# Kernel optimization log

Measured on AMD Instinct MI355X. Metric: run time of the kernel, lower is better.

## Reference

```python
import jax, jax.numpy as jnp
import numpy as np

EPS = 1e-5

def _gn(x, w, b):
    # GroupNorm with 1 group on [N, C]: normalize each row over C, then affine.
    mu = jnp.mean(x, axis=-1, keepdims=True)
    var = jnp.mean((x - mu) ** 2, axis=-1, keepdims=True)
    return (x - mu) * jax.lax.rsqrt(var + EPS) * w + b

def setup_inputs() -> dict:
    key = jax.random.key(0)
    ks = jax.random.split(key, 24)
    N_AGT, N_CTX, E, D, NC = 50000, 100000, 500000, 128, 2
    s = 0.05  # weight init scale
    inp = {
        "agts": jax.random.normal(ks[0], (N_AGT, D), jnp.float32),
        "ctx": jax.random.normal(ks[1], (N_CTX, D), jnp.float32),
        "agt_ctrs": jax.random.normal(ks[2], (N_AGT, NC), jnp.float32),
        "ctx_ctrs": jax.random.normal(ks[3], (N_CTX, NC), jnp.float32),
        "hi": jax.random.randint(ks[4], (E,), 0, N_AGT, jnp.int32),
        "wi": jax.random.randint(ks[5], (E,), 0, N_CTX, jnp.int32),
        # dist MLP: Linear(2->128, bias) + ReLU, then Linear(128->128 no bias)+GN+ReLU
        "Wd1": jax.random.normal(ks[6], (D, NC), jnp.float32) * s,
        "bd1": jnp.zeros((D,), jnp.float32),
        "Wd2": jax.random.normal(ks[7], (D, D), jnp.float32) * s,
        "gd2w": jnp.ones((D,), jnp.float32), "gd2b": jnp.zeros((D,), jnp.float32),
        # query: Linear(128->128 no bias)+GN+ReLU
        "Wq": jax.random.normal(ks[8], (D, D), jnp.float32) * s,
        "gqw": jnp.ones((D,), jnp.float32), "gqb": jnp.zeros((D,), jnp.float32),
        # ctx MLP: Linear(384->128 no bias)+GN+ReLU, then Linear(128->128 no bias)
        "Wc1": jax.random.normal(ks[9], (D, 3 * D), jnp.float32) * s,
        "gc1w": jnp.ones((D,), jnp.float32), "gc1b": jnp.zeros((D,), jnp.float32),
        "Wc2": jax.random.normal(ks[10], (D, D), jnp.float32) * s,
        # agt linear (no bias), post-scatter GN, final Linear(no bias)+GN
        "Wa": jax.random.normal(ks[11], (D, D), jnp.float32) * s,
        "gnw": jnp.ones((D,), jnp.float32), "gnb": jnp.zeros((D,), jnp.float32),
        "Wl": jax.random.normal(ks[12], (D, D), jnp.float32) * s,
        "glw": jnp.ones((D,), jnp.float32), "glb": jnp.zeros((D,), jnp.float32),
    }
    return inp

def reference(agts, ctx, agt_ctrs, ctx_ctrs, hi, wi,
              Wd1, bd1, Wd2, gd2w, gd2b, Wq, gqw, gqb,
              Wc1, gc1w, gc1b, Wc2, Wa, gnw, gnb, Wl, glw, glb):
    res = agts
    # dist branch: relative center offsets of edges -> MLP
    d = agt_ctrs[hi] - ctx_ctrs[wi]                    # [E, 2]
    d = jax.nn.relu(d @ Wd1.T + bd1)                   # [E, 128]
    d = jax.nn.relu(_gn(d @ Wd2.T, gd2w, gd2b))        # [E, 128]
    # query branch: gathered agent features
    q = jax.nn.relu(_gn(agts[hi] @ Wq.T, gqw, gqb))    # [E, 128]
    # ctx branch: concat(dist, query, gathered ctx) -> MLP
    c = jnp.concatenate([d, q, ctx[wi]], axis=1)       # [E, 384]
    c = jax.nn.relu(_gn(c @ Wc1.T, gc1w, gc1b))        # [E, 128]
    c = c @ Wc2.T                                      # [E, 128]
    # scatter-add messages back to agents
    a = agts @ Wa.T
    a = a.at[hi].add(c)
    a = jax.nn.relu(_gn(a, gnw, gnb))
    a = _gn(a @ Wl.T, glw, glb)
    return jax.nn.relu(a + res)
```

## Files before the change

### kernel.cpp

```cpp
#include <hip/hip_runtime.h>
#include <hip/hip_bf16.h>

#define D 128
#define TM 64
#define APITCH 136
#define WSLICE 16384

typedef __attribute__((ext_vector_type(8))) short short8;
typedef __attribute__((ext_vector_type(4))) float f32x4;
typedef __attribute__((ext_vector_type(2))) float f32x2;

__device__ __forceinline__ short f2bf(float f) {
    union { float f; unsigned u; } v; v.f = f;
    unsigned r = v.u + 0x7fffu + ((v.u >> 16) & 1u);
    return (short)(r >> 16);
}
__device__ __forceinline__ float bflo(unsigned v) {
    union { unsigned u; float f; } t; t.u = v << 16; return t.f;
}
__device__ __forceinline__ float bfhi(unsigned v) {
    union { unsigned u; float f; } t; t.u = v & 0xffff0000u; return t.f;
}
__device__ __forceinline__ unsigned pkbf(float a, float b) {
    return (unsigned)(unsigned short)f2bf(a) | ((unsigned)(unsigned short)f2bf(b) << 16);
}

struct TileLDS {
    short A[TM * APITCH];
    f32x2 red[TM][4][4];
    f32x2 mr[TM];
    int hi_s[TM];
    int wi_s[TM];
};

struct WPA { const float* src[8]; int pitch[8]; int coloff[8]; };

__global__ __launch_bounds__(256)
void k_wprep(WPA a, short* __restrict__ wf) {
    int slice = blockIdx.x & 7, chunk = blockIdx.x >> 3;
    int tid = threadIdx.x, lane = tid & 63;
    int slot = chunk * 4 + (tid >> 6);
    int w = slot >> 3, t = (slot >> 2) & 1, ks = slot & 3;
    int lr = lane & 15, kh = lane >> 4;
    const float* src = a.src[slice];
    int row = w * 32 + t * 16 + lr;
    int col0 = a.coloff[slice] + ks * 32 + kh * 8;
    short8 v;
#pragma unroll
    for (int j = 0; j < 8; ++j) v[j] = f2bf(src[(size_t)row * a.pitch[slice] + col0 + j]);
    *(short8*)&wf[(size_t)slice * WSLICE + ((size_t)slot * 64 + lane) * 8] = v;
}

__device__ __forceinline__ void load_wset_pre(const short* wf, int slice, int w, int lane,
                                              short8 frag[2][4]) {
    const short8* p = (const short8*)(wf + (size_t)slice * WSLICE);
#pragma unroll
    for (int t = 0; t < 2; ++t)
#pragma unroll
        for (int ks = 0; ks < 4; ++ks)
            frag[t][ks] = p[((w * 2 + t) * 4 + ks) * 64 + lane];
}

__device__ __forceinline__ void wave_gemm(const short* A, const short8 frag[2][4],
                                          int lr, int kh, f32x4 acc[4][2]) {
#pragma unroll
    for (int mt = 0; mt < 4; ++mt)
#pragma unroll
        for (int t = 0; t < 2; ++t)
            acc[mt][t] = (f32x4){0.f, 0.f, 0.f, 0.f};
#pragma unroll
    for (int ks = 0; ks < 4; ++ks) {
        short8 a[4];
#pragma unroll
        for (int mt = 0; mt < 4; ++mt)
            a[mt] = *(const short8*)&A[(mt * 16 + lr) * APITCH + ks * 32 + kh * 8];
#pragma unroll
        for (int mt = 0; mt < 4; ++mt)
#pragma unroll
            for (int t = 0; t < 2; ++t)
                acc[mt][t] = __builtin_amdgcn_mfma_f32_16x16x32_bf16(a[mt], frag[t][ks], acc[mt][t], 0, 0, 0);
    }
}

__device__ __forceinline__ void store_acc_global(float* Y, long rbase, int M,
                                                 const f32x4 acc[4][2], int lane, int w) {
    int lr = lane & 15, hh = lane >> 4;
#pragma unroll
    for (int mt = 0; mt < 4; ++mt)
#pragma unroll
        for (int t = 0; t < 2; ++t)
#pragma unroll
            for (int r = 0; r < 4; ++r) {
                int row = mt * 16 + hh * 4 + r;
                if (rbase + row < M)
                    Y[(size_t)(rbase + row) * D + w * 32 + t * 16 + lr] = acc[mt][t][r];
            }
}

__device__ __forceinline__ void store_acc_pk(unsigned* Y, long rbase, int M,
                                             const f32x4 acc[4][2], int lane, int w) {
    int lr = lane & 15, hh = lane >> 4;
#pragma unroll
    for (int mt = 0; mt < 4; ++mt)
#pragma unroll
        for (int r = 0; r < 4; ++r) {
            int row = mt * 16 + hh * 4 + r;
            if (rbase + row < M)
                Y[(size_t)(rbase + row) * 64 + w * 16 + lr] = pkbf(acc[mt][0][r], acc[mt][1][r]);
        }
}

__device__ __forceinline__ void gn_stats(TileLDS& L, const f32x4 acc[4][2],
                                         int tid, int lane, int w) {
    int lr = lane & 15, hh = lane >> 4;
#pragma unroll
    for (int mt = 0; mt < 4; ++mt)
#pragma unroll
        for (int r = 0; r < 4; ++r) {
            float s = acc[mt][0][r] + acc[mt][1][r];
            float q = acc[mt][0][r] * acc[mt][0][r] + acc[mt][1][r] * acc[mt][1][r];
            s += __shfl_xor(s, 1); q += __shfl_xor(q, 1);
            s += __shfl_xor(s, 2); q += __shfl_xor(q, 2);
            if ((lr & 3) == mt) {
                int row = mt * 16 + hh * 4 + r;
                L.red[row][w][lr >> 2] = (f32x2){s, q};
            }
        }
    __syncthreads();
    if (tid < TM) {
        float s = 0.f, q = 0.f;
        const f32x2* p = (const f32x2*)L.red[tid];
#pragma unroll
        for (int i = 0; i < 16; ++i) { f32x2 v = p[i]; s += v[0]; q += v[1]; }
        float mu = s * (1.f / 128.f);
        float var = q * (1.f / 128.f) - mu * mu;
        L.mr[tid] = (f32x2){mu, rsqrtf(var + 1e-5f)};
    }
    __syncthreads();
}

__device__ __forceinline__ void gn_reg(TileLDS& L, const f32x4 acc[4][2],
                                       float gw0, float gb0, float gw1, float gb1,
                                       int tid, int lane, int w) {
    gn_stats(L, acc, tid, lane, w);
    int lr = lane & 15, hh = lane >> 4, n0 = w * 32;
#pragma unroll
    for (int mt = 0; mt < 4; ++mt)
#pragma unroll
        for (int r = 0; r < 4; ++r) {
            int row = mt * 16 + hh * 4 + r;
            f32x2 m = L.mr[row];
            float v0 = (acc[mt][0][r] - m[0]) * m[1] * gw0 + gb0;
            float v1 = (acc[mt][1][r] - m[0]) * m[1] * gw1 + gb1;
            L.A[row * APITCH + n0 + lr]      = f2bf(fmaxf(v0, 0.f));
            L.A[row * APITCH + n0 + 16 + lr] = f2bf(fmaxf(v1, 0.f));
        }
    __syncthreads();
}

__device__ __forceinline__ void stage_rows_to_A(TileLDS& L, const float* X, long rbase, int M, int tid) {
#pragma unroll
    for (int it = 0; it < 8; ++it) {
        int chunk = tid + it * 256;
        int row = chunk >> 5, c4 = chunk & 31;
        long r = rbase + row;
        float4 v = (r < M) ? *(const float4*)&X[(size_t)r * D + c4 * 4] : make_float4(0.f, 0.f, 0.f, 0.f);
        short* a = &L.A[row * APITCH + c4 * 4];
        a[0] = f2bf(v.x); a[1] = f2bf(v.y); a[2] = f2bf(v.z); a[3] = f2bf(v.w);
    }
}

__global__ void k_hist(const int* __restrict__ hi, int* __restrict__ cnt, int E) {
    int i = blockIdx.x * 256 + threadIdx.x;
    if (i < E) atomicAdd(&cnt[hi[i]], 1);
}

__global__ void k_scan(const int* __restrict__ cnt, int* __restrict__ offs,
                       int* __restrict__ cursor, int n) {
    __shared__ int wsum[4];
    __shared__ int carry_s;
    int tid = threadIdx.x, lane = tid & 63, w = tid >> 6;
    if (tid == 0) carry_s = 0;
    __syncthreads();
    for (int base = 0; base < n; base += 256) {
        int i = base + tid;
        int v = (i < n) ? cnt[i] : 0;
        int x = v;
#pragma unroll
        for (int d = 1; d < 64; d <<= 1) {
            int t = __shfl_up(x, d);
            if (lane >= d) x += t;
        }
        if (lane == 63) wsum[w] = x;
        __syncthreads();
        int woff = 0;
        for (int j = 0; j < w; ++j) woff += wsum[j];
        int carry = carry_s;
        int excl = carry + woff + x - v;
        if (i < n) { offs[i] = excl; cursor[i] = excl; }
        __syncthreads();
        if (tid == 255) carry_s = carry + woff + x;
        __syncthreads();
    }
    if (tid == 0) offs[n] = carry_s;
}

__global__ void k_fill(const int* __restrict__ hi, const int* __restrict__ wi,
                       int* __restrict__ cursor,
                       int* __restrict__ hi_srt, int* __restrict__ wi_srt, int E) {
    int i = blockIdx.x * 256 + threadIdx.x;
    if (i < E) {
        int h = hi[i];
        int p = atomicAdd(&cursor[h], 1);
        hi_srt[p] = h;
        wi_srt[p] = wi[i];
    }
}

__global__ __launch_bounds__(256, 3)
void k_qpath(const float* __restrict__ agts, const short* __restrict__ wf,
             const float* __restrict__ gqw, const float* __restrict__ gqb,
             unsigned* __restrict__ qp32, float* __restrict__ abuf, int M, int ntiles) {
    __shared__ TileLDS L;
    int tid = threadIdx.x;
    int lane = tid & 63, w = tid >> 6;
    int lr = lane & 15, kh = lane >> 4;
    int n0 = w * 32;
    short8 fa[2][4], fq[2][4], fcq[2][4];
    load_wset_pre(wf, 0, w, lane, fa);
    load_wset_pre(wf, 1, w, lane, fq);
    load_wset_pre(wf, 3, w, lane, fcq);
    float gw0 = gqw[n0 + lr], gw1 = gqw[n0 + 16 + lr];
    float gb0 = gqb[n0 + lr], gb1 = gqb[n0 + 16 + lr];

    for (int tile = blockIdx.x; tile < ntiles; tile += gridDim.x) {
        long rbase = (long)tile * TM;
        stage_rows_to_A(L, agts, rbase, M, tid);
        __syncthreads();
        f32x4 acc[4][2];
        wave_gemm(L.A, fa, lr, kh, acc);
        store_acc_global(abuf, rbase, M, acc, lane, w);
        wave_gemm(L.A, fq, lr, kh, acc);
        gn_reg(L, acc, gw0, gb0, gw1, gb1, tid, lane, w);
        wave_gemm(L.A, fcq, lr, kh, acc);
        store_acc_pk(qp32, rbase, M, acc, lane, w);
        __syncthreads();
    }
}

__global__ __launch_bounds__(256, 4)
void k_ctx(const float* __restrict__ ctx, const short* __restrict__ wf,
           unsigned* __restrict__ cp32, int M, int ntiles) {
    __shared__ TileLDS L;
    int tid = threadIdx.x;
    int lane = tid & 63, w = tid >> 6;
    int lr = lane & 15, kh = lane >> 4;
    short8 fc[2][4];
    load_wset_pre(wf, 4, w, lane, fc);
    for (int tile = blockIdx.x; tile < ntiles; tile += gridDim.x) {
        long rbase = (long)tile * TM;
        stage_rows_to_A(L, ctx, rbase, M, tid);
        __syncthreads();
        f32x4 acc[4][2];
        wave_gemm(L.A, fc, lr, kh, acc);
        store_acc_pk(cp32, rbase, M, acc, lane, w);
        __syncthreads();
    }
}

__global__ __launch_bounds__(256, 3)
void k_edge(const float* __restrict__ agt_ctrs, const float* __restrict__ ctx_ctrs,
            const int* __restrict__ hi_srt, const int* __restrict__ wi_srt,
            const float* __restrict__ Wd1, const float* __restrict__ bd1,
            const short* __restrict__ wf,
            const float* __restrict__ gd2w, const float* __restrict__ gd2b,
            const float* __restrict__ gc1w, const float* __restrict__ gc1b,
            const unsigned* __restrict__ qp32, const unsigned* __restrict__ cp32,
            unsigned* __restrict__ ebuf32, int E, int ntiles) {
    __shared__ TileLDS L;
    int tid = threadIdx.x;
    int lane = tid & 63, w = tid >> 6;
    int lr = lane & 15, kh = lane >> 4;
    int n0 = w * 32;
    short8 fd2[2][4], fc1[2][4], fc2[2][4];
    load_wset_pre(wf, 5, w, lane, fd2);
    load_wset_pre(wf, 2, w, lane, fc1);
    load_wset_pre(wf, 6, w, lane, fc2);
    float g2w0 = gd2w[n0 + lr], g2w1 = gd2w[n0 + 16 + lr];
    float g2b0 = gd2b[n0 + lr], g2b1 = gd2b[n0 + 16 + lr];
    float g1w0 = gc1w[n0 + lr], g1w1 = gc1w[n0 + 16 + lr];
    float g1b0 = gc1b[n0 + lr], g1b1 = gc1b[n0 + 16 + lr];

    for (int tile = blockIdx.x; tile < ntiles; tile += gridDim.x) {
        long ebase = (long)tile * TM;
        if (tid < TM) {
            long e = ebase + tid;
            L.hi_s[tid] = (e < E) ? hi_srt[e] : 0;
            L.wi_s[tid] = (e < E) ? wi_srt[e] : 0;
        }
        {
            int row = tid >> 2, q4 = tid & 3;
            long e = ebase + row;
            bool valid = e < E;
            float dd0 = 0.f, dd1 = 0.f;
            if (valid) {
                int h = hi_srt[e], c = wi_srt[e];
                dd0 = agt_ctrs[h * 2 + 0] - ctx_ctrs[c * 2 + 0];
                dd1 = agt_ctrs[h * 2 + 1] - ctx_ctrs[c * 2 + 1];
            }
#pragma unroll
            for (int cb = 0; cb < 4; ++cb) {
                short8 ov;
#pragma unroll
                for (int j = 0; j < 8; ++j) {
                    int c = q4 * 32 + cb * 8 + j;
                    float v = valid ? fmaxf(Wd1[c * 2 + 0] * dd0 + Wd1[c * 2 + 1] * dd1 + bd1[c], 0.f) : 0.f;
                    ov[j] = f2bf(v);
                }
                *(short8*)&L.A[row * APITCH + q4 * 32 + cb * 8] = ov;
            }
        }
        __syncthreads();
        f32x4 acc[4][2];
        wave_gemm(L.A, fd2, lr, kh, acc);
        gn_reg(L, acc, g2w0, g2b0, g2w1, g2b1, tid, lane, w);
        wave_gemm(L.A, fc1, lr, kh, acc);
#pragma unroll
        for (int mt = 0; mt < 4; ++mt)
#pragma unroll
            for (int r = 0; r < 4; ++r) {
                int row = mt * 16 + kh * 4 + r;
                unsigned vq = qp32[(size_t)L.hi_s[row] * 64 + w * 16 + lr];
                unsigned vc = cp32[(size_t)L.wi_s[row] * 64 + w * 16 + lr];
                acc[mt][0][r] += bflo(vq) + bflo(vc);
                acc[mt][1][r] += bfhi(vq) + bfhi(vc);
            }
        gn_reg(L, acc, g1w0, g1b0, g1w1, g1b1, tid, lane, w);
        wave_gemm(L.A, fc2, lr, kh, acc);
#pragma unroll
        for (int mt = 0; mt < 4; ++mt)
#pragma unroll
            for (int r = 0; r < 4; ++r) {
                int erow = mt * 16 + kh * 4 + r;
                long e = ebase + erow;
                if (e < E)
                    ebuf32[(size_t)e * 64 + w * 16 + lr] = pkbf(acc[mt][0][r], acc[mt][1][r]);
            }
        __syncthreads();
    }
}

__global__ __launch_bounds__(256, 4)
void k_final(const float* __restrict__ abuf, const float* __restrict__ agts,
             const unsigned* __restrict__ ebuf32, const int* __restrict__ offs,
             const short* __restrict__ wf,
             const float* __restrict__ gnw, const float* __restrict__ gnb,
             const float* __restrict__ glw, const float* __restrict__ glb,
             float* __restrict__ out, int M, int ntiles) {
    __shared__ TileLDS L;
    int tid = threadIdx.x;
    int lane = tid & 63, w = tid >> 6;
    int lr = lane & 15, kh = lane >> 4;
    int n0 = w * 32;
    short8 fl[2][4];
    load_wset_pre(wf, 7, w, lane, fl);
    float gw0 = glw[n0 + lr], gw1 = glw[n0 + 16 + lr];
    float gb0 = glb[n0 + lr], gb1 = glb[n0 + 16 + lr];

    for (int tile = blockIdx.x; tile < ntiles; tile += gridDim.x) {
        long rbase = (long)tile * TM;
        int row = tid >> 2, q4 = tid & 3;
        long r = rbase + row;
        float x[32];
        {
            const float4* src = (const float4*)(abuf + (size_t)r * D + q4 * 32);
#pragma unroll
            for (int i = 0; i < 8; ++i) {
                float4 v = (r < M) ? src[i] : make_float4(0.f, 0.f, 0.f, 0.f);
                x[i * 4 + 0] = v.x; x[i * 4 + 1] = v.y; x[i * 4 + 2] = v.z; x[i * 4 + 3] = v.w;
            }
            if (r < M) {
                int s0 = offs[r], e1 = offs[r + 1];
                for (int p = s0; p < e1; ++p) {
                    const unsigned* er = ebuf32 + (size_t)p * 64 + q4 * 16;
#pragma unroll
                    for (int j = 0; j < 16; ++j) {
                        unsigned v = er[j];
                        x[j]      += bflo(v);
                        x[16 + j] += bfhi(v);
                    }
                }
            }
            float s = 0.f, q = 0.f;
#pragma unroll
            for (int i = 0; i < 32; ++i) { s += x[i]; q += x[i] * x[i]; }
            L.red[row][q4][0] = (f32x2){s, q};
        }
        __syncthreads();
        if (tid < TM) {
            float s = 0.f, q = 0.f;
#pragma unroll
            for (int i = 0; i < 4; ++i) { f32x2 v = L.red[tid][i][0]; s += v[0]; q += v[1]; }
            float mu = s * (1.f / 128.f);
            float var = q * (1.f / 128.f) - mu * mu;
            L.mr[tid] = (f32x2){mu, rsqrtf(var + 1e-5f)};
        }
        __syncthreads();
        {
            f32x2 m = L.mr[row];
#pragma unroll
            for (int cb = 0; cb < 4; ++cb) {
                short8 ov;
#pragma unroll
                for (int j = 0; j < 8; ++j) {
                    int c = q4 * 32 + cb * 8 + j;
                    float v = (x[cb * 8 + j] - m[0]) * m[1] * gnw[c] + gnb[c];
                    ov[j] = f2bf(fmaxf(v, 0.f));
                }
                *(short8*)&L.A[row * APITCH + q4 * 32 + cb * 8] = ov;
            }
        }
        __syncthreads();
        f32x4 acc[4][2];
        wave_gemm(L.A, fl, lr, kh, acc);
        gn_stats(L, acc, tid, lane, w);
#pragma unroll
        for (int mt = 0; mt < 4; ++mt)
#pragma unroll
            for (int rr = 0; rr < 4; ++rr) {
                int orow = mt * 16 + kh * 4 + rr;
                long gr = rbase + orow;
                if (gr < M) {
                    f32x2 m = L.mr[orow];
                    float v0 = (acc[mt][0][rr] - m[0]) * m[1] * gw0 + gb0;
                    float v1 = (acc[mt][1][rr] - m[0]) * m[1] * gw1 + gb1;
                    v0 += agts[(size_t)gr * D + n0 + lr];
                    v1 += agts[(size_t)gr * D + n0 + 16 + lr];
                    out[(size_t)gr * D + n0 + lr]      = fmaxf(v0, 0.f);
                    out[(size_t)gr * D + n0 + 16 + lr] = fmaxf(v1, 0.f);
                }
            }
        __syncthreads();
    }
}

extern "C" void kernel_launch(void* const* d_in, const int* in_sizes, int n_in,
                              void* d_out, int out_size, void* d_ws, size_t ws_size,
                              hipStream_t stream) {
    const float* agts     = (const float*)d_in[0];
    const float* ctx      = (const float*)d_in[1];
    const float* agt_ctrs = (const float*)d_in[2];
    const float* ctx_ctrs = (const float*)d_in[3];
    const int*   hi       = (const int*)d_in[4];
    const int*   wi       = (const int*)d_in[5];
    const float* Wd1 = (const float*)d_in[6];
    const float* bd1 = (const float*)d_in[7];
    const float* Wd2 = (const float*)d_in[8];
    const float* gd2w = (const float*)d_in[9];
    const float* gd2b = (const float*)d_in[10];
    const float* Wq  = (const float*)d_in[11];
    const float* gqw = (const float*)d_in[12];
    const float* gqb = (const float*)d_in[13];
    const float* Wc1 = (const float*)d_in[14];
    const float* gc1w = (const float*)d_in[15];
    const float* gc1b = (const float*)d_in[16];
    const float* Wc2 = (const float*)d_in[17];
    const float* Wa  = (const float*)d_in[18];
    const float* gnw = (const float*)d_in[19];
    const float* gnb = (const float*)d_in[20];
    const float* Wl  = (const float*)d_in[21];
    const float* glw = (const float*)d_in[22];
    const float* glb = (const float*)d_in[23];

    int N_AGT = in_sizes[0] / D;
    int N_CTX = in_sizes[1] / D;
    int E     = in_sizes[4];
    float* out = (float*)d_out;

    short*    wf     = (short*)d_ws;
    unsigned* qp32   = (unsigned*)(wf + 8 * WSLICE);
    unsigned* cp32   = qp32 + (size_t)N_AGT * 64;
    float*    abuf   = (float*)(cp32 + (size_t)N_CTX * 64);
    unsigned* ebuf32 = (unsigned*)(abuf + (size_t)N_AGT * D);
    int*      cnt    = (int*)(ebuf32 + (size_t)E * 64);
    int*      offs   = cnt + N_AGT;
    int*      cursor = offs + N_AGT + 1;
    int*      hi_srt = cursor + N_AGT;
    int*      wi_srt = hi_srt + E;

    int tq = (N_AGT + TM - 1) / TM;
    int tc = (N_CTX + TM - 1) / TM;
    int te = (E + TM - 1) / TM;
    int ge = (E + 255) / 256;
    int gq = tq < 768 ? tq : 768;
    int gc = tc < 768 ? tc : 768;
    int gE = te < 1536 ? te : 1536;
    int gf = tq < 768 ? tq : 768;

    WPA wpa;
    wpa.src[0] = Wa;  wpa.pitch[0] = 128; wpa.coloff[0] = 0;
    wpa.src[1] = Wq;  wpa.pitch[1] = 128; wpa.coloff[1] = 0;
    wpa.src[2] = Wc1; wpa.pitch[2] = 384; wpa.coloff[2] = 0;
    wpa.src[3] = Wc1; wpa.pitch[3] = 384; wpa.coloff[3] = 128;
    wpa.src[4] = Wc1; wpa.pitch[4] = 384; wpa.coloff[4] = 256;
    wpa.src[5] = Wd2; wpa.pitch[5] = 128; wpa.coloff[5] = 0;
    wpa.src[6] = Wc2; wpa.pitch[6] = 128; wpa.coloff[6] = 0;
    wpa.src[7] = Wl;  wpa.pitch[7] = 128; wpa.coloff[7] = 0;

    hipMemsetAsync(cnt, 0, (size_t)N_AGT * sizeof(int), stream);
    k_wprep<<<64, 256, 0, stream>>>(wpa, wf);
    k_hist<<<ge, 256, 0, stream>>>(hi, cnt, E);
    k_scan<<<1, 256, 0, stream>>>(cnt, offs, cursor, N_AGT);
    k_fill<<<ge, 256, 0, stream>>>(hi, wi, cursor, hi_srt, wi_srt, E);

    k_qpath<<<gq, 256, 0, stream>>>(agts, wf, gqw, gqb, qp32, abuf, N_AGT, tq);
    k_ctx<<<gc, 256, 0, stream>>>(ctx, wf, cp32, N_CTX, tc);
    k_edge<<<gE, 256, 0, stream>>>(agt_ctrs, ctx_ctrs, hi_srt, wi_srt, Wd1, bd1, wf,
                                   gd2w, gd2b, gc1w, gc1b, qp32, cp32, ebuf32, E, te);
    k_final<<<gf, 256, 0, stream>>>(abuf, agts, ebuf32, offs, wf,
                                    gnw, gnb, glw, glb, out, N_AGT, tq);
}
```

Measured before the change: 859.4 us.

## Coalesce edge gathers via LDS staging and assign contiguous tiles per XCD

The edge kernel now gathers each edge's q/ctx projection rows with full-row coalesced loads (one lane per 32-bit word), issued before the GEMMs so their latency overlaps compute. The rows are then staged through LDS and re-read in MFMA accumulator layout, replacing the scattered per-element global gathers. Tiles are also partitioned into contiguous chunks per XCD (blockIdx & 7) to improve L2 locality of the sorted edges, and the grid is fixed at 2048 blocks. This adds four extra barriers and 32 live registers per thread for the staged rows, which may reduce occupancy.

Result: slower. 991.5 us (+15.4%).

```diff
diff --git a/kernel.cpp b/kernel.cpp
--- a/kernel.cpp
+++ b/kernel.cpp
@@ -4,6 +4,7 @@
 #define D 128
 #define TM 64
 #define APITCH 136
+#define UPITCH 68
 #define WSLICE 16384
 
 typedef __attribute__((ext_vector_type(8))) short short8;
@@ -291,7 +292,15 @@
     float g1w0 = gc1w[n0 + lr], g1w1 = gc1w[n0 + 16 + lr];
     float g1b0 = gc1b[n0 + lr], g1b1 = gc1b[n0 + 16 + lr];
 
-    for (int tile = blockIdx.x; tile < ntiles; tile += gridDim.x) {
+    int xcd = blockIdx.x & 7, slot = blockIdx.x >> 3;
+    int nslots = gridDim.x >> 3;
+    int q = ntiles >> 3, r = ntiles & 7;
+    int cstart = xcd * q + (xcd < r ? xcd : r);
+    int csize = q + (xcd < r ? 1 : 0);
+
+    unsigned* Abuf = (unsigned*)L.A;
+
+    for (int tile = cstart + slot; tile < cstart + csize; tile += nslots) {
         long ebase = (long)tile * TM;
         if (tid < TM) {
             long e = ebase + tid;
@@ -321,30 +330,52 @@
             }
         }
         __syncthreads();
+        unsigned qreg[16], creg[16];
+#pragma unroll
+        for (int i = 0; i < 16; ++i) {
+            qreg[i] = qp32[(size_t)L.hi_s[w * 16 + i] * 64 + lane];
+            creg[i] = cp32[(size_t)L.wi_s[w * 16 + i] * 64 + lane];
+        }
         f32x4 acc[4][2];
         wave_gemm(L.A, fd2, lr, kh, acc);
         gn_reg(L, acc, g2w0, g2b0, g2w1, g2b1, tid, lane, w);
         wave_gemm(L.A, fc1, lr, kh, acc);
+        __syncthreads();
+#pragma unroll
+        for (int i = 0; i < 16; ++i) Abuf[(w * 16 + i) * UPITCH + lane] = qreg[i];
+        __syncthreads();
 #pragma unroll
         for (int mt = 0; mt < 4; ++mt)
 #pragma unroll
-            for (int r = 0; r < 4; ++r) {
-                int row = mt * 16 + kh * 4 + r;
-                unsigned vq = qp32[(size_t)L.hi_s[row] * 64 + w * 16 + lr];
-                unsigned vc = cp32[(size_t)L.wi_s[row] * 64 + w * 16 + lr];
-                acc[mt][0][r] += bflo(vq) + bflo(vc);
-                acc[mt][1][r] += bfhi(vq) + bfhi(vc);
+            for (int r2 = 0; r2 < 4; ++r2) {
+                int row = mt * 16 + kh * 4 + r2;
+                unsigned v = Abuf[row * UPITCH + w * 16 + lr];
+                acc[mt][0][r2] += bflo(v);
+                acc[mt][1][r2] += bfhi(v);
+            }
+        __syncthreads();
+#pragma unroll
+        for (int i = 0; i < 16; ++i) Abuf[(w * 16 + i) * UPITCH + lane] = creg[i];
+        __syncthreads();
+#pragma unroll
+        for (int mt = 0; mt < 4; ++mt)
+#pragma unroll
+            for (int r2 = 0; r2 < 4; ++r2) {
+                int row = mt * 16 + kh * 4 + r2;
+                unsigned v = Abuf[row * UPITCH + w * 16 + lr];
+                acc[mt][0][r2] += bflo(v);
+                acc[mt][1][r2] += bfhi(v);
             }
         gn_reg(L, acc, g1w0, g1b0, g1w1, g1b1, tid, lane, w);
         wave_gemm(L.A, fc2, lr, kh, acc);
 #pragma unroll
         for (int mt = 0; mt < 4; ++mt)
 #pragma unroll
-            for (int r = 0; r < 4; ++r) {
-                int erow = mt * 16 + kh * 4 + r;
+            for (int r2 = 0; r2 < 4; ++r2) {
+                int erow = mt * 16 + kh * 4 + r2;
                 long e = ebase + erow;
                 if (e < E)
-                    ebuf32[(size_t)e * 64 + w * 16 + lr] = pkbf(acc[mt][0][r], acc[mt][1][r]);
+                    ebuf32[(size_t)e * 64 + w * 16 + lr] = pkbf(acc[mt][0][r2], acc[mt][1][r2]);
             }
         __syncthreads();
     }
@@ -494,7 +525,6 @@
     int ge = (E + 255) / 256;
     int gq = tq < 768 ? tq : 768;
     int gc = tc < 768 ? tc : 768;
-    int gE = te < 1536 ? te : 1536;
     int gf = tq < 768 ? tq : 768;
 
     WPA wpa;
@@ -515,8 +545,8 @@
 
     k_qpath<<<gq, 256, 0, stream>>>(agts, wf, gqw, gqb, qp32, abuf, N_AGT, tq);
     k_ctx<<<gc, 256, 0, stream>>>(ctx, wf, cp32, N_CTX, tc);
-    k_edge<<<gE, 256, 0, stream>>>(agt_ctrs, ctx_ctrs, hi_srt, wi_srt, Wd1, bd1, wf,
-                                   gd2w, gd2b, gc1w, gc1b, qp32, cp32, ebuf32, E, te);
+    k_edge<<<2048, 256, 0, stream>>>(agt_ctrs, ctx_ctrs, hi_srt, wi_srt, Wd1, bd1, wf,
+                                     gd2w, gd2b, gc1w, gc1b, qp32, cp32, ebuf32, E, te);
     k_final<<<gf, 256, 0, stream>>>(abuf, agts, ebuf32, offs, wf,
                                     gnw, gnb, glw, glb, out, N_AGT, tq);
 }
```
